# Performance work log

Measured on AMD Instinct MI355X. Metric: run time of the kernel, lower is better.

Reference implementation:

```python
import jax, jax.numpy as jnp
import numpy as np

N_NODES = 50000
N_EDGES = 800000
IN_DIM = 128
HIDDEN = 128
NUM_CLASSES = 64
NEG_SLOPE = 0.2


def setup_inputs() -> dict:
    key = jax.random.key(0)
    ks = jax.random.split(key, 12)
    x = jax.random.normal(ks[0], (N_NODES, IN_DIM), dtype=jnp.float32)
    src = jax.random.randint(ks[1], (N_EDGES,), 0, N_NODES, dtype=jnp.int64)
    dst = jax.random.randint(ks[2], (N_EDGES,), 0, N_NODES, dtype=jnp.int64)
    def glorot(k, shape):
        fan_in, fan_out = shape[0], shape[-1]
        s = jnp.sqrt(2.0 / (fan_in + fan_out)).astype(jnp.float32)
        return jax.random.normal(k, shape, dtype=jnp.float32) * s
    return {
        "x": x, "src": src, "dst": dst,
        # GATConv params (1 head, no bias, no residual)
        "W_gat": glorot(ks[3], (IN_DIM, HIDDEN)),
        "attn_l": glorot(ks[4], (HIDDEN,)),
        "attn_r": glorot(ks[5], (HIDDEN,)),
        # GraphConv params (norm='none', bias=True)
        "W1": glorot(ks[6], (HIDDEN, HIDDEN)),
        "b1": jnp.zeros((HIDDEN,), dtype=jnp.float32),
        "W2": glorot(ks[7], (HIDDEN, HIDDEN)),
        "b2": jnp.zeros((HIDDEN,), dtype=jnp.float32),
        "Wc": glorot(ks[8], (HIDDEN, NUM_CLASSES)),
        "bc": jnp.zeros((NUM_CLASSES,), dtype=jnp.float32),
    }


def reference(x, src, dst, W_gat, attn_l, attn_r, W1, b1, W2, b2, Wc, bc):
    N = x.shape[0]
    # --- GATConv, single head, eval mode (dropout=0) ---
    h = x @ W_gat                      # (N, H)
    el = h @ attn_l                    # (N,)
    er = h @ attn_r                    # (N,)
    e = jax.nn.leaky_relu(el[src] + er[dst], negative_slope=NEG_SLOPE)  # (E,)
    # edge softmax over incoming edges of each dst node
    emax = jax.ops.segment_max(e, dst, num_segments=N)
    ee = jnp.exp(e - emax[dst])
    esum = jax.ops.segment_sum(ee, dst, num_segments=N)
    alpha = ee / esum[dst]             # (E,) attention = reused edge weights
    h1 = jax.ops.segment_sum(h[src] * alpha[:, None], dst, num_segments=N)
    h1 = jax.nn.elu(h1)                # GATConv activation

    # --- GraphConv (norm='none') with edge_weight = alpha ---
    def gconv(hin, W, b):
        hp = hin @ W                                   # project (order is math-equivalent)
        agg = jax.ops.segment_sum(hp[src] * alpha[:, None], dst, num_segments=N)
        return agg + b

    h2 = gconv(h1, W1, b1)
    h3 = gconv(h2, W2, b2)
    logits = gconv(h3, Wc, bc)         # (N, num_classes)
    return logits
```

## Files before the change

### kernel.cpp

```cpp
#include <hip/hip_runtime.h>
#include <hip/hip_fp16.h>
#include <math.h>

#define N_NODES 50000
#define N_EDGES 800000
#define PAD_EDGES (N_EDGES + 8 * N_NODES)

typedef _Float16 half8 __attribute__((ext_vector_type(8)));
typedef float floatx16 __attribute__((ext_vector_type(16)));

__global__ __launch_bounds__(256) void prep_a_k(const float* __restrict__ Wg,
                                                const float* __restrict__ W1,
                                                const float* __restrict__ W2,
                                                const float* __restrict__ b1,
                                                __half* __restrict__ Wg_hl,
                                                float* __restrict__ W12,
                                                float* __restrict__ c12) {
  int e = blockIdx.x * 256 + threadIdx.x;
  if (e < 16384) {
    _Float16* o = (_Float16*)Wg_hl;
    int k = e >> 7, n = e & 127;
    float w = Wg[k * 128 + n];
    _Float16 hi = (_Float16)w;
    float lo = w - (float)hi;
    int oi = (((k >> 3) * 128 + n) << 3) | (k & 7);
    o[oi] = hi;
    o[16384 + oi] = (_Float16)lo;
  } else if (e < 32768) {
    int local = e - 16384;
    int k = local >> 7, n = local & 127;
    float acc = 0.f;
    for (int j = 0; j < 128; ++j) acc = fmaf(W1[k * 128 + j], W2[j * 128 + n], acc);
    W12[k * 128 + n] = acc;
  } else if (e < 32896) {
    int n = e - 32768;
    float acc = 0.f;
    for (int j = 0; j < 128; ++j) acc = fmaf(b1[j], W2[j * 128 + n], acc);
    c12[n] = acc;
  }
}

__global__ __launch_bounds__(256) void prepP_k(const float* __restrict__ W12,
                                               const float* __restrict__ c12,
                                               const float* __restrict__ Wc,
                                               const float* __restrict__ b2,
                                               __half* __restrict__ WPhl,
                                               float* __restrict__ c1,
                                               float* __restrict__ c2) {
  int e = blockIdx.x * 256 + threadIdx.x;
  _Float16* o = (_Float16*)WPhl;
  if (e < 8192) {
    int k = e >> 6, n = e & 63;
    float acc = 0.f;
    for (int j = 0; j < 128; ++j) acc = fmaf(W12[k * 128 + j], Wc[j * 64 + n], acc);
    _Float16 hi = (_Float16)acc;
    float lo = acc - (float)hi;
    int oi = (((k >> 3) * 64 + n) << 3) | (k & 7);
    o[oi] = hi;
    o[8192 + oi] = (_Float16)lo;
  } else if (e < 8256) {
    int n = e - 8192;
    float acc = 0.f;
    for (int j = 0; j < 128; ++j) acc = fmaf(c12[j], Wc[j * 64 + n], acc);
    c1[n] = acc;
  } else if (e < 8320) {
    int n = e - 8256;
    float acc = 0.f;
    for (int j = 0; j < 128; ++j) acc = fmaf(b2[j], Wc[j * 64 + n], acc);
    c2[n] = acc;
  }
}

template <int NCOL, bool A16, bool ELR>
__global__ __launch_bounds__(256) void mgemm_k(const void* __restrict__ Ap,
                                               const __half* __restrict__ Whl,
                                               __half* __restrict__ C16, int M,
                                               const float* __restrict__ al,
                                               const float* __restrict__ ar,
                                               float* __restrict__ el,
                                               float* __restrict__ er) {
  __shared__ __half Al[16][129][8];
  const int tid  = threadIdx.x;
  const int row0 = blockIdx.x * 128;
  const int lane = tid & 63;
  const int lane31 = lane & 31;
  const int q = lane >> 5;
  const int r = tid >> 6;

  if (A16) {
    const uint4* A8 = (const uint4*)Ap;
    #pragma unroll
    for (int i = 0; i < 8; ++i) {
      int idx = tid + i * 256;
      int row = idx >> 4, c = idx & 15;
      int grow = row0 + row;
      uint4 v = make_uint4(0u, 0u, 0u, 0u);
      if (grow < M) v = A8[grow * 16 + c];
      *reinterpret_cast<uint4*>(&Al[c][row][0]) = v;
    }
  } else {
    const float4* A4 = (const float4*)Ap;
    #pragma unroll
    for (int i = 0; i < 8; ++i) {
      int idx = tid + i * 256;
      int row = idx >> 4, c = idx & 15;
      int grow = row0 + row;
      half8 hv = {};
      if (grow < M) {
        float4 a0 = A4[grow * 32 + c * 2];
        float4 a1 = A4[grow * 32 + c * 2 + 1];
        hv[0] = (_Float16)a0.x; hv[1] = (_Float16)a0.y;
        hv[2] = (_Float16)a0.z; hv[3] = (_Float16)a0.w;
        hv[4] = (_Float16)a1.x; hv[5] = (_Float16)a1.y;
        hv[6] = (_Float16)a1.z; hv[7] = (_Float16)a1.w;
      }
      *reinterpret_cast<half8*>(&Al[c][row][0]) = hv;
    }
  }
  __syncthreads();

  half8 afr[8];
  #pragma unroll
  for (int s = 0; s < 8; ++s)
    afr[s] = *reinterpret_cast<const half8*>(&Al[2 * s + q][r * 32 + lane31][0]);

  const half8* B8 = reinterpret_cast<const half8*>(Whl);
  const int KN8 = 16 * NCOL;

  float elp[16], erp[16];
  if (ELR) {
    #pragma unroll
    for (int i = 0; i < 16; ++i) { elp[i] = 0.f; erp[i] = 0.f; }
  }

  #pragma unroll
  for (int tc = 0; tc < NCOL / 32; ++tc) {
    floatx16 acc = {};
    int nbase = tc * 32 + lane31;
    #pragma unroll
    for (int s = 0; s < 8; ++s) {
      int ci = (2 * s + q) * NCOL + nbase;
      half8 bl = B8[KN8 + ci];
      half8 bh = B8[ci];
      acc = __builtin_amdgcn_mfma_f32_32x32x16_f16(afr[s], bl, acc, 0, 0, 0);
      acc = __builtin_amdgcn_mfma_f32_32x32x16_f16(afr[s], bh, acc, 0, 0, 0);
    }
    if (ELR) {
      float alv = al[nbase], arv = ar[nbase];
      #pragma unroll
      for (int i = 0; i < 16; ++i) {
        elp[i] = fmaf(acc[i], alv, elp[i]);
        erp[i] = fmaf(acc[i], arv, erp[i]);
      }
    }
    #pragma unroll
    for (int i = 0; i < 16; ++i) {
      int rl = (i & 3) + 8 * (i >> 2) + 4 * q;
      int grow = row0 + r * 32 + rl;
      if (grow < M) C16[grow * NCOL + nbase] = __float2half(acc[i]);
    }
  }

  if (ELR) {
    #pragma unroll
    for (int off = 1; off <= 16; off <<= 1) {
      #pragma unroll
      for (int i = 0; i < 16; ++i) {
        elp[i] += __shfl_xor(elp[i], off);
        erp[i] += __shfl_xor(erp[i], off);
      }
    }
    if (lane31 == 0) {
      #pragma unroll
      for (int i = 0; i < 16; ++i) {
        int rl = (i & 3) + 8 * (i >> 2) + 4 * q;
        int grow = row0 + r * 32 + rl;
        if (grow < M) { el[grow] = elp[i]; er[grow] = erp[i]; }
      }
    }
  }
}

__global__ __launch_bounds__(256) void hist_k(const int* __restrict__ dst,
                                              int* __restrict__ deg,
                                              int* __restrict__ rank, int E) {
  int e = blockIdx.x * 256 + threadIdx.x;
  if (e < E) rank[e] = atomicAdd(&deg[dst[e]], 1);
}

__global__ __launch_bounds__(256) void scan1_k(const int* __restrict__ deg,
                                               int* __restrict__ offs,
                                               int* __restrict__ bsum, int N) {
  __shared__ int s[256];
  int t = threadIdx.x;
  int i = blockIdx.x * 256 + t;
  int v = 0;
  if (i < N) {
    int d = deg[i];
    v = (d + 7) & ~7;
    if (v < 8) v = 8;
  }
  s[t] = v;
  __syncthreads();
  for (int o = 1; o < 256; o <<= 1) {
    int add = (t >= o) ? s[t - o] : 0;
    __syncthreads();
    s[t] += add;
    __syncthreads();
  }
  if (i < N) offs[i] = s[t] - v;
  if (t == 255) bsum[blockIdx.x] = s[255];
}

__global__ __launch_bounds__(256) void scan2_k(int* __restrict__ bsum, int nb) {
  __shared__ int s[256];
  int t = threadIdx.x;
  int v = (t < nb) ? bsum[t] : 0;
  s[t] = v;
  __syncthreads();
  for (int o = 1; o < 256; o <<= 1) {
    int add = (t >= o) ? s[t - o] : 0;
    __syncthreads();
    s[t] += add;
    __syncthreads();
  }
  if (t < nb) bsum[t] = s[t] - v;
}

__global__ __launch_bounds__(256) void scan3_k(int* __restrict__ offs,
                                               const int* __restrict__ deg,
                                               const int* __restrict__ bsum,
                                               const float* __restrict__ el,
                                               float2* __restrict__ el2, int N) {
  int i = blockIdx.x * 256 + threadIdx.x;
  if (i < N) {
    int o = offs[i] + bsum[blockIdx.x];
    offs[i] = o;
    int d = deg[i];
    el2[i] = make_float2(el[i], (d > 0) ? 1.f : 0.f);
    if (i == N - 1) {
      int pd = (d + 7) & ~7;
      if (pd < 8) pd = 8;
      offs[N] = o + pd;
    }
  }
}

__global__ __launch_bounds__(256) void scatter_k(const int* __restrict__ src,
                                                 const int* __restrict__ dst,
                                                 const int* __restrict__ offs,
                                                 const int* __restrict__ rank,
                                                 int* __restrict__ csr_src, int E) {
  int e = blockIdx.x * 256 + threadIdx.x;
  if (e < E) {
    csr_src[offs[dst[e]] + rank[e]] = src[e];
  }
}

__device__ inline void fma8(float2 acc[4], uint4 u, float a) {
  __half2* h = reinterpret_cast<__half2*>(&u);
  #pragma unroll
  for (int j = 0; j < 4; ++j) {
    float2 f = __half22float2(h[j]);
    acc[j].x = fmaf(a, f.x, acc[j].x);
    acc[j].y = fmaf(a, f.y, acc[j].y);
  }
}

__global__ __launch_bounds__(256) void aggsm_k(const int* __restrict__ offs,
                                               const int* __restrict__ deg,
                                               const int* __restrict__ csr_src,
                                               const float2* __restrict__ el2,
                                               const float* __restrict__ er,
                                               int2* __restrict__ meta,
                                               float* __restrict__ t,
                                               const __half* __restrict__ hp,
                                               __half* __restrict__ out, int N) {
  __shared__ int2 lmeta[4][64];
  int wv   = threadIdx.x >> 6;
  int w    = (blockIdx.x * 256 + threadIdx.x) >> 6;
  int lane = threadIdx.x & 63;
  if (w >= N) return;
  int o0   = offs[w];
  int pcnt = offs[w + 1] - o0;
  int cnt  = deg[w];
  int q  = lane >> 4;
  int fl = lane & 15;
  const uint4* hpq = reinterpret_cast<const uint4*>(hp);

  if (cnt <= 64) {
    bool valid = lane < cnt;
    float erv = er[w];
    int s = 0;
    float ev = -3.4e38f, flag = 0.f;
    if (valid) {
      s = csr_src[o0 + lane];
      float2 e2 = el2[s];
      float e0 = e2.x + erv;
      ev = (e0 >= 0.f) ? e0 : 0.2f * e0;
      flag = e2.y;
    }
    float m = ev;
    #pragma unroll
    for (int off = 32; off; off >>= 1) m = fmaxf(m, __shfl_xor(m, off));
    float ee = valid ? __expf(ev - m) : 0.f;
    float sum = ee, tp = ee * flag;
    #pragma unroll
    for (int off = 32; off; off >>= 1) {
      sum += __shfl_xor(sum, off);
      tp  += __shfl_xor(tp, off);
    }
    float inv = (cnt > 0) ? 1.f / sum : 0.f;
    int2 mm = make_int2(0, 0);
    if (valid) mm = make_int2(s * 16, __float_as_int(ee * inv));
    if (lane < pcnt) meta[o0 + lane] = mm;
    lmeta[wv][lane] = mm;
    if (lane == 0) t[w] = tp * inv;
  } else {
    float erv = er[w];
    float m = -3.4e38f;
    for (int i = lane; i < cnt; i += 64) {
      int s = csr_src[o0 + i];
      float2 e2 = el2[s];
      float ev = e2.x + erv;
      ev = (ev >= 0.f) ? ev : 0.2f * ev;
      m = fmaxf(m, ev);
    }
    #pragma unroll
    for (int off = 32; off; off >>= 1) m = fmaxf(m, __shfl_xor(m, off));
    float sum = 0.f, tacc = 0.f;
    int myS = 0; float myE = 0.f;
    for (int i = lane; i < cnt; i += 64) {
      int s = csr_src[o0 + i];
      float2 e2 = el2[s];
      float ev = e2.x + erv;
      ev = (ev >= 0.f) ? ev : 0.2f * ev;
      float ee = __expf(ev - m);
      meta[o0 + i] = make_int2(s * 16, __float_as_int(ee));
      sum += ee;
      tacc += ee * e2.y;
      if (i == lane) { myS = s; myE = ee; }
    }
    #pragma unroll
    for (int off = 32; off; off >>= 1) {
      sum  += __shfl_xor(sum, off);
      tacc += __shfl_xor(tacc, off);
    }
    float inv = 1.f / sum;
    if (lane == 0) t[w] = tacc * inv;
    for (int i = lane; i < cnt; i += 64) {
      int2 mm = meta[o0 + i];
      meta[o0 + i] = make_int2(mm.x, __float_as_int(__int_as_float(mm.y) * inv));
    }
    for (int i = cnt + lane; i < pcnt; i += 64) meta[o0 + i] = make_int2(0, 0);
    lmeta[wv][lane] = make_int2(myS * 16, __float_as_int(myE * inv));
  }

  float2 acc0[4] = {}, acc1[4] = {};
  int pc = pcnt < 64 ? pcnt : 64;
  int2 mA = lmeta[wv][q], mB = lmeta[wv][4 + q];
  for (int base = 8; base < pc; base += 8) {
    int2 nA = lmeta[wv][base + q], nB = lmeta[wv][base + 4 + q];
    uint4 vA = hpq[mA.x + fl], vB = hpq[mB.x + fl];
    fma8(acc0, vA, __int_as_float(mA.y));
    fma8(acc1, vB, __int_as_float(mB.y));
    mA = nA; mB = nB;
  }
  {
    uint4 vA = hpq[mA.x + fl], vB = hpq[mB.x + fl];
    fma8(acc0, vA, __int_as_float(mA.y));
    fma8(acc1, vB, __int_as_float(mB.y));
  }
  for (int p = o0 + 64 + q; p < o0 + pcnt; p += 4) {
    int2 mm = meta[p];
    fma8(acc0, hpq[mm.x + fl], __int_as_float(mm.y));
  }
  #pragma unroll
  for (int j = 0; j < 4; ++j) { acc0[j].x += acc1[j].x; acc0[j].y += acc1[j].y; }
  #pragma unroll
  for (int off = 16; off <= 32; off <<= 1) {
    #pragma unroll
    for (int j = 0; j < 4; ++j) {
      acc0[j].x += __shfl_xor(acc0[j].x, off);
      acc0[j].y += __shfl_xor(acc0[j].y, off);
    }
  }
  if (q == 0) {
    float o8[8];
    #pragma unroll
    for (int j = 0; j < 4; ++j) { o8[2 * j] = acc0[j].x; o8[2 * j + 1] = acc0[j].y; }
    #pragma unroll
    for (int j = 0; j < 8; ++j) o8[j] = (o8[j] > 0.f) ? o8[j] : (__expf(o8[j]) - 1.f);
    __half2 p0 = __floats2half2_rn(o8[0], o8[1]);
    __half2 p1 = __floats2half2_rn(o8[2], o8[3]);
    __half2 p2 = __floats2half2_rn(o8[4], o8[5]);
    __half2 p3 = __floats2half2_rn(o8[6], o8[7]);
    uint4 pk;
    pk.x = *reinterpret_cast<unsigned*>(&p0);
    pk.y = *reinterpret_cast<unsigned*>(&p1);
    pk.z = *reinterpret_cast<unsigned*>(&p2);
    pk.w = *reinterpret_cast<unsigned*>(&p3);
    *reinterpret_cast<uint4*>(&out[w * 128 + fl * 8]) = pk;
  }
}

template <bool FINAL>
__global__ __launch_bounds__(256) void agg64v_k(const int* __restrict__ offs,
                                                const int2* __restrict__ meta,
                                                const __half* __restrict__ zp,
                                                const float* __restrict__ t,
                                                const int* __restrict__ deg,
                                                const float* __restrict__ c1,
                                                const float* __restrict__ c2,
                                                const float* __restrict__ bc,
                                                void* __restrict__ outp, int N) {
  int w    = (blockIdx.x * 256 + threadIdx.x) >> 6;
  int lane = threadIdx.x & 63;
  if (w >= N) return;
  int o0 = offs[w], o1 = offs[w + 1];
  int o   = lane >> 3;
  int fl  = lane & 7;
  const uint4* hpq = reinterpret_cast<const uint4*>(zp);

  float2 acc0[4] = {};
  int p = o0 + o;
  int2 mA = meta[p];
  for (; p + 8 < o1; p += 8) {
    int2 nA = meta[p + 8];
    uint4 vA = hpq[(mA.x >> 1) + fl];
    fma8(acc0, vA, __int_as_float(mA.y));
    mA = nA;
  }
  {
    uint4 vA = hpq[(mA.x >> 1) + fl];
    fma8(acc0, vA, __int_as_float(mA.y));
  }
  #pragma unroll
  for (int off = 8; off <= 32; off <<= 1) {
    #pragma unroll
    for (int j = 0; j < 4; ++j) {
      acc0[j].x += __shfl_xor(acc0[j].x, off);
      acc0[j].y += __shfl_xor(acc0[j].y, off);
    }
  }
  if (o == 0) {
    float o8[8];
    #pragma unroll
    for (int j = 0; j < 4; ++j) { o8[2 * j] = acc0[j].x; o8[2 * j + 1] = acc0[j].y; }
    if (FINAL) {
      float tw = t[w];
      float dw = (deg[w] > 0) ? 1.f : 0.f;
      float4 a0 = reinterpret_cast<const float4*>(c1)[fl * 2];
      float4 a1 = reinterpret_cast<const float4*>(c1)[fl * 2 + 1];
      float4 d0 = reinterpret_cast<const float4*>(c2)[fl * 2];
      float4 d1 = reinterpret_cast<const float4*>(c2)[fl * 2 + 1];
      float4 b0 = reinterpret_cast<const float4*>(bc)[fl * 2];
      float4 b1v = reinterpret_cast<const float4*>(bc)[fl * 2 + 1];
      o8[0] += tw * a0.x + dw * d0.x + b0.x;
      o8[1] += tw * a0.y + dw * d0.y + b0.y;
      o8[2] += tw * a0.z + dw * d0.z + b0.z;
      o8[3] += tw * a0.w + dw * d0.w + b0.w;
      o8[4] += tw * a1.x + dw * d1.x + b1v.x;
      o8[5] += tw * a1.y + dw * d1.y + b1v.y;
      o8[6] += tw * a1.z + dw * d1.z + b1v.z;
      o8[7] += tw * a1.w + dw * d1.w + b1v.w;
      float4* of = reinterpret_cast<float4*>(outp);
      of[w * 16 + fl * 2]     = make_float4(o8[0], o8[1], o8[2], o8[3]);
      of[w * 16 + fl * 2 + 1] = make_float4(o8[4], o8[5], o8[6], o8[7]);
    } else {
      __half2 p0 = __floats2half2_rn(o8[0], o8[1]);
      __half2 p1 = __floats2half2_rn(o8[2], o8[3]);
      __half2 p2 = __floats2half2_rn(o8[4], o8[5]);
      __half2 p3 = __floats2half2_rn(o8[6], o8[7]);
      uint4 pk;
      pk.x = *reinterpret_cast<unsigned*>(&p0);
      pk.y = *reinterpret_cast<unsigned*>(&p1);
      pk.z = *reinterpret_cast<unsigned*>(&p2);
      pk.w = *reinterpret_cast<unsigned*>(&p3);
      reinterpret_cast<uint4*>(outp)[w * 8 + fl] = pk;
    }
  }
}

extern "C" void kernel_launch(void* const* d_in, const int* in_sizes, int n_in,
                              void* d_out, int out_size, void* d_ws, size_t ws_size,
                              hipStream_t stream) {
  const float* x      = (const float*)d_in[0];
  const int*   src    = (const int*)d_in[1];
  const int*   dst    = (const int*)d_in[2];
  const float* W_gat  = (const float*)d_in[3];
  const float* attn_l = (const float*)d_in[4];
  const float* attn_r = (const float*)d_in[5];
  const float* W1     = (const float*)d_in[6];
  const float* b1     = (const float*)d_in[7];
  const float* W2     = (const float*)d_in[8];
  const float* b2     = (const float*)d_in[9];
  const float* Wc     = (const float*)d_in[10];
  const float* bc     = (const float*)d_in[11];
  float* out = (float*)d_out;

  char* ws = (char*)d_ws;
  size_t off = 0;
  auto walloc = [&](size_t bytes) -> void* {
    void* p = ws + off;
    off += (bytes + 255) & ~size_t(255);
    return p;
  };
  __half* P16     = (__half*)walloc((size_t)N_NODES * 128 * 2);
  __half* F16     = (__half*)walloc((size_t)N_NODES * 128 * 2);
  float*  el      = (float*)walloc((size_t)N_NODES * 4);
  float*  er      = (float*)walloc((size_t)N_NODES * 4);
  float2* el2     = (float2*)walloc((size_t)N_NODES * 8);
  float*  tbuf    = (float*)walloc((size_t)N_NODES * 4);
  int*    deg     = (int*)walloc((size_t)N_NODES * 4);
  int*    offs    = (int*)walloc((size_t)(N_NODES + 1) * 4);
  int*    rank    = (int*)walloc((size_t)N_EDGES * 4);
  int*    csr_src = (int*)walloc((size_t)PAD_EDGES * 4);
  int2*   meta    = (int2*)walloc((size_t)PAD_EDGES * 8);
  int*    bsum    = (int*)walloc(1024);
  __half* Wg_hl   = (__half*)walloc((size_t)32768 * 2);
  __half* WP_hl   = (__half*)walloc((size_t)16384 * 2);
  float*  W12     = (float*)walloc((size_t)16384 * 4);
  float*  c12     = (float*)walloc((size_t)128 * 4);
  float*  c1      = (float*)walloc((size_t)64 * 4);
  float*  c2      = (float*)walloc((size_t)64 * 4);

  hipMemsetAsync(deg, 0, (size_t)N_NODES * 4, stream);

  const dim3 blk(256);
  const int nwave_blocks = (N_NODES + 3) / 4;
  const int nedge_blocks = (N_EDGES + 255) / 256;
  const int nscan_blocks = (N_NODES + 255) / 256;
  const int ngemm_blocks = (N_NODES + 127) / 128;

  prep_a_k<<<dim3(129), blk, 0, stream>>>(W_gat, W1, W2, b1, Wg_hl, W12, c12);
  prepP_k<<<dim3(33), blk, 0, stream>>>(W12, c12, Wc, b2, WP_hl, c1, c2);

  mgemm_k<128, false, true><<<dim3(ngemm_blocks), blk, 0, stream>>>(
      x, Wg_hl, P16, N_NODES, attn_l, attn_r, el, er);

  hist_k<<<dim3(nedge_blocks), blk, 0, stream>>>(dst, deg, rank, N_EDGES);
  scan1_k<<<dim3(nscan_blocks), blk, 0, stream>>>(deg, offs, bsum, N_NODES);
  scan2_k<<<dim3(1), blk, 0, stream>>>(bsum, nscan_blocks);
  scan3_k<<<dim3(nscan_blocks), blk, 0, stream>>>(offs, deg, bsum, el, el2, N_NODES);
  scatter_k<<<dim3(nedge_blocks), blk, 0, stream>>>(src, dst, offs, rank, csr_src, N_EDGES);

  aggsm_k<<<dim3(nwave_blocks), blk, 0, stream>>>(offs, deg, csr_src, el2, er, meta, tbuf, P16, F16, N_NODES);
  mgemm_k<64, true, false><<<dim3(ngemm_blocks), blk, 0, stream>>>(
      F16, WP_hl, P16, N_NODES, nullptr, nullptr, nullptr, nullptr);
  agg64v_k<false><<<dim3(nwave_blocks), blk, 0, stream>>>(offs, meta, P16, nullptr, nullptr, nullptr, nullptr, nullptr, F16, N_NODES);
  agg64v_k<false><<<dim3(nwave_blocks), blk, 0, stream>>>(offs, meta, F16, nullptr, nullptr, nullptr, nullptr, nullptr, P16, N_NODES);
  agg64v_k<true><<<dim3(nwave_blocks), blk, 0, stream>>>(offs, meta, P16, tbuf, deg, c1, c2, bc, out, N_NODES);
}
```

Measured before the change: 289.0 us.

## Fuse weight prep and CSR build into one persistent kernel with grid barriers

Merges the two weight-prep kernels, histogram, three scan kernels and scatter into a single persistent kernel of 196 blocks that synchronises phases with atomic grid barriers, removing six kernel launches and their gaps. The el/degree-flag packing moves into the first GEMM epilogue, which now reads deg, so that GEMM must run after the CSR build. Per-node padding grows from 8 to 16 so agg64v can process two edges per lane per iteration with two accumulators for more memory-level parallelism. The grid barrier assumes all 196 blocks are co-resident, and the larger padding adds wasted zero-weight edge work.

```diff
diff --git a/kernel.cpp b/kernel.cpp
--- a/kernel.cpp
+++ b/kernel.cpp
@@ -4,71 +4,145 @@
 
 #define N_NODES 50000
 #define N_EDGES 800000
-#define PAD_EDGES (N_EDGES + 8 * N_NODES)
+#define PAD_EDGES (N_EDGES + 16 * N_NODES)
+#define NB_COOP 196
 
 typedef _Float16 half8 __attribute__((ext_vector_type(8)));
 typedef float floatx16 __attribute__((ext_vector_type(16)));
 
-__global__ __launch_bounds__(256) void prep_a_k(const float* __restrict__ Wg,
-                                                const float* __restrict__ W1,
-                                                const float* __restrict__ W2,
-                                                const float* __restrict__ b1,
-                                                __half* __restrict__ Wg_hl,
-                                                float* __restrict__ W12,
-                                                float* __restrict__ c12) {
-  int e = blockIdx.x * 256 + threadIdx.x;
-  if (e < 16384) {
-    _Float16* o = (_Float16*)Wg_hl;
-    int k = e >> 7, n = e & 127;
-    float w = Wg[k * 128 + n];
-    _Float16 hi = (_Float16)w;
-    float lo = w - (float)hi;
-    int oi = (((k >> 3) * 128 + n) << 3) | (k & 7);
-    o[oi] = hi;
-    o[16384 + oi] = (_Float16)lo;
-  } else if (e < 32768) {
-    int local = e - 16384;
-    int k = local >> 7, n = local & 127;
-    float acc = 0.f;
-    for (int j = 0; j < 128; ++j) acc = fmaf(W1[k * 128 + j], W2[j * 128 + n], acc);
-    W12[k * 128 + n] = acc;
-  } else if (e < 32896) {
-    int n = e - 32768;
-    float acc = 0.f;
-    for (int j = 0; j < 128; ++j) acc = fmaf(b1[j], W2[j * 128 + n], acc);
-    c12[n] = acc;
-  }
-}
-
-__global__ __launch_bounds__(256) void prepP_k(const float* __restrict__ W12,
-                                               const float* __restrict__ c12,
-                                               const float* __restrict__ Wc,
-                                               const float* __restrict__ b2,
-                                               __half* __restrict__ WPhl,
-                                               float* __restrict__ c1,
-                                               float* __restrict__ c2) {
-  int e = blockIdx.x * 256 + threadIdx.x;
-  _Float16* o = (_Float16*)WPhl;
-  if (e < 8192) {
-    int k = e >> 6, n = e & 63;
-    float acc = 0.f;
-    for (int j = 0; j < 128; ++j) acc = fmaf(W12[k * 128 + j], Wc[j * 64 + n], acc);
-    _Float16 hi = (_Float16)acc;
-    float lo = acc - (float)hi;
-    int oi = (((k >> 3) * 64 + n) << 3) | (k & 7);
-    o[oi] = hi;
-    o[8192 + oi] = (_Float16)lo;
-  } else if (e < 8256) {
-    int n = e - 8192;
-    float acc = 0.f;
-    for (int j = 0; j < 128; ++j) acc = fmaf(c12[j], Wc[j * 64 + n], acc);
-    c1[n] = acc;
-  } else if (e < 8320) {
-    int n = e - 8256;
-    float acc = 0.f;
-    for (int j = 0; j < 128; ++j) acc = fmaf(b2[j], Wc[j * 64 + n], acc);
-    c2[n] = acc;
-  }
+__device__ inline void gridbar(int* bar, int ph) {
+  __syncthreads();
+  if (threadIdx.x == 0) {
+    __hip_atomic_fetch_add(&bar[ph], 1, __ATOMIC_RELEASE, __HIP_MEMORY_SCOPE_AGENT);
+    while (__hip_atomic_load(&bar[ph], __ATOMIC_ACQUIRE, __HIP_MEMORY_SCOPE_AGENT) < NB_COOP)
+      __builtin_amdgcn_s_sleep(8);
+  }
+  __syncthreads();
+}
+
+__global__ __launch_bounds__(256) void coop_k(const int* __restrict__ src,
+                                              const int* __restrict__ dst,
+                                              const float* __restrict__ Wg,
+                                              const float* __restrict__ W1,
+                                              const float* __restrict__ W2,
+                                              const float* __restrict__ b1,
+                                              const float* __restrict__ Wc,
+                                              const float* __restrict__ b2,
+                                              int* __restrict__ deg,
+                                              int* __restrict__ rank,
+                                              int* __restrict__ offs,
+                                              int* __restrict__ csr_src,
+                                              int* __restrict__ bsum,
+                                              int* __restrict__ bsum2,
+                                              __half* __restrict__ Wg_hl,
+                                              float* __restrict__ W12,
+                                              float* __restrict__ c12,
+                                              __half* __restrict__ WPhl,
+                                              float* __restrict__ c1,
+                                              float* __restrict__ c2,
+                                              int* __restrict__ bar) {
+  __shared__ int s[256];
+  const int tid = threadIdx.x;
+  const int gt = blockIdx.x * 256 + tid;
+  const int GT = NB_COOP * 256;
+
+  for (int e = gt; e < 32896; e += GT) {
+    if (e < 16384) {
+      _Float16* o = (_Float16*)Wg_hl;
+      int k = e >> 7, n = e & 127;
+      float w = Wg[k * 128 + n];
+      _Float16 hi = (_Float16)w;
+      float lo = w - (float)hi;
+      int oi = (((k >> 3) * 128 + n) << 3) | (k & 7);
+      o[oi] = hi;
+      o[16384 + oi] = (_Float16)lo;
+    } else if (e < 32768) {
+      int local = e - 16384;
+      int k = local >> 7, n = local & 127;
+      float acc = 0.f;
+      for (int j = 0; j < 128; ++j) acc = fmaf(W1[k * 128 + j], W2[j * 128 + n], acc);
+      W12[k * 128 + n] = acc;
+    } else {
+      int n = e - 32768;
+      float acc = 0.f;
+      for (int j = 0; j < 128; ++j) acc = fmaf(b1[j], W2[j * 128 + n], acc);
+      c12[n] = acc;
+    }
+  }
+  gridbar(bar, 0);
+
+  for (int e = gt; e < N_EDGES; e += GT) rank[e] = atomicAdd(&deg[dst[e]], 1);
+  for (int e = gt; e < 8320; e += GT) {
+    _Float16* o = (_Float16*)WPhl;
+    if (e < 8192) {
+      int k = e >> 6, n = e & 63;
+      float acc = 0.f;
+      for (int j = 0; j < 128; ++j) acc = fmaf(W12[k * 128 + j], Wc[j * 64 + n], acc);
+      _Float16 hi = (_Float16)acc;
+      float lo = acc - (float)hi;
+      int oi = (((k >> 3) * 64 + n) << 3) | (k & 7);
+      o[oi] = hi;
+      o[8192 + oi] = (_Float16)lo;
+    } else if (e < 8256) {
+      int n = e - 8192;
+      float acc = 0.f;
+      for (int j = 0; j < 128; ++j) acc = fmaf(c12[j], Wc[j * 64 + n], acc);
+      c1[n] = acc;
+    } else {
+      int n = e - 8256;
+      float acc = 0.f;
+      for (int j = 0; j < 128; ++j) acc = fmaf(b2[j], Wc[j * 64 + n], acc);
+      c2[n] = acc;
+    }
+  }
+  gridbar(bar, 1);
+
+  const int i = gt;
+  int v = 0;
+  if (i < N_NODES) {
+    int d = deg[i];
+    v = (d + 15) & ~15;
+    if (v < 16) v = 16;
+  }
+  s[tid] = v;
+  __syncthreads();
+  for (int o = 1; o < 256; o <<= 1) {
+    int add = (tid >= o) ? s[tid - o] : 0;
+    __syncthreads();
+    s[tid] += add;
+    __syncthreads();
+  }
+  if (i < N_NODES) offs[i] = s[tid] - v;
+  if (tid == 255) bsum[blockIdx.x] = s[255];
+  gridbar(bar, 2);
+
+  if (blockIdx.x == 0) {
+    int bv = (tid < NB_COOP) ? bsum[tid] : 0;
+    s[tid] = bv;
+    __syncthreads();
+    for (int o = 1; o < 256; o <<= 1) {
+      int add = (tid >= o) ? s[tid - o] : 0;
+      __syncthreads();
+      s[tid] += add;
+      __syncthreads();
+    }
+    if (tid < NB_COOP) bsum2[tid] = s[tid] - bv;
+  }
+  gridbar(bar, 3);
+
+  if (i < N_NODES) {
+    int o = offs[i] + bsum2[blockIdx.x];
+    offs[i] = o;
+    if (i == N_NODES - 1) {
+      int d = deg[i];
+      int pd = (d + 15) & ~15;
+      if (pd < 16) pd = 16;
+      offs[N_NODES] = o + pd;
+    }
+  }
+  gridbar(bar, 4);
+
+  for (int e = gt; e < N_EDGES; e += GT) csr_src[offs[dst[e]] + rank[e]] = src[e];
 }
 
 template <int NCOL, bool A16, bool ELR>
@@ -77,8 +151,9 @@
                                                __half* __restrict__ C16, int M,
                                                const float* __restrict__ al,
                                                const float* __restrict__ ar,
-                                               float* __restrict__ el,
-                                               float* __restrict__ er) {
+                                               float2* __restrict__ el2,
+                                               float* __restrict__ er,
+                                               const int* __restrict__ deg) {
   __shared__ __half Al[16][129][8];
   const int tid  = threadIdx.x;
   const int row0 = blockIdx.x * 128;
@@ -175,85 +250,12 @@
       for (int i = 0; i < 16; ++i) {
         int rl = (i & 3) + 8 * (i >> 2) + 4 * q;
         int grow = row0 + r * 32 + rl;
-        if (grow < M) { el[grow] = elp[i]; er[grow] = erp[i]; }
+        if (grow < M) {
+          er[grow] = erp[i];
+          el2[grow] = make_float2(elp[i], (deg[grow] > 0) ? 1.f : 0.f);
+        }
       }
     }
-  }
-}
-
-__global__ __launch_bounds__(256) void hist_k(const int* __restrict__ dst,
-                                              int* __restrict__ deg,
-                                              int* __restrict__ rank, int E) {
-  int e = blockIdx.x * 256 + threadIdx.x;
-  if (e < E) rank[e] = atomicAdd(&deg[dst[e]], 1);
-}
-
-__global__ __launch_bounds__(256) void scan1_k(const int* __restrict__ deg,
-                                               int* __restrict__ offs,
-                                               int* __restrict__ bsum, int N) {
-  __shared__ int s[256];
-  int t = threadIdx.x;
-  int i = blockIdx.x * 256 + t;
-  int v = 0;
-  if (i < N) {
-    int d = deg[i];
-    v = (d + 7) & ~7;
-    if (v < 8) v = 8;
-  }
-  s[t] = v;
-  __syncthreads();
-  for (int o = 1; o < 256; o <<= 1) {
-    int add = (t >= o) ? s[t - o] : 0;
-    __syncthreads();
-    s[t] += add;
-    __syncthreads();
-  }
-  if (i < N) offs[i] = s[t] - v;
-  if (t == 255) bsum[blockIdx.x] = s[255];
-}
-
-__global__ __launch_bounds__(256) void scan2_k(int* __restrict__ bsum, int nb) {
-  __shared__ int s[256];
-  int t = threadIdx.x;
-  int v = (t < nb) ? bsum[t] : 0;
-  s[t] = v;
-  __syncthreads();
-  for (int o = 1; o < 256; o <<= 1) {
-    int add = (t >= o) ? s[t - o] : 0;
-    __syncthreads();
-    s[t] += add;
-    __syncthreads();
-  }
-  if (t < nb) bsum[t] = s[t] - v;
-}
-
-__global__ __launch_bounds__(256) void scan3_k(int* __restrict__ offs,
-                                               const int* __restrict__ deg,
-                                               const int* __restrict__ bsum,
-                                               const float* __restrict__ el,
-                                               float2* __restrict__ el2, int N) {
-  int i = blockIdx.x * 256 + threadIdx.x;
-  if (i < N) {
-    int o = offs[i] + bsum[blockIdx.x];
-    offs[i] = o;
-    int d = deg[i];
-    el2[i] = make_float2(el[i], (d > 0) ? 1.f : 0.f);
-    if (i == N - 1) {
-      int pd = (d + 7) & ~7;
-      if (pd < 8) pd = 8;
-      offs[N] = o + pd;
-    }
-  }
-}
-
-__global__ __launch_bounds__(256) void scatter_k(const int* __restrict__ src,
-                                                 const int* __restrict__ dst,
-                                                 const int* __restrict__ offs,
-                                                 const int* __restrict__ rank,
-                                                 int* __restrict__ csr_src, int E) {
-  int e = blockIdx.x * 256 + threadIdx.x;
-  if (e < E) {
-    csr_src[offs[dst[e]] + rank[e]] = src[e];
   }
 }
 
@@ -422,19 +424,25 @@
   int fl  = lane & 7;
   const uint4* hpq = reinterpret_cast<const uint4*>(zp);
 
-  float2 acc0[4] = {};
+  float2 acc0[4] = {}, acc1[4] = {};
   int p = o0 + o;
-  int2 mA = meta[p];
-  for (; p + 8 < o1; p += 8) {
-    int2 nA = meta[p + 8];
+  int2 mA = meta[p], mB = meta[p + 8];
+  for (; p + 16 < o1; p += 16) {
+    int2 nA = meta[p + 16], nB = meta[p + 24];
     uint4 vA = hpq[(mA.x >> 1) + fl];
+    uint4 vB = hpq[(mB.x >> 1) + fl];
     fma8(acc0, vA, __int_as_float(mA.y));
-    mA = nA;
+    fma8(acc1, vB, __int_as_float(mB.y));
+    mA = nA; mB = nB;
   }
   {
     uint4 vA = hpq[(mA.x >> 1) + fl];
+    uint4 vB = hpq[(mB.x >> 1) + fl];
     fma8(acc0, vA, __int_as_float(mA.y));
-  }
+    fma8(acc1, vB, __int_as_float(mB.y));
+  }
+  #pragma unroll
+  for (int j = 0; j < 4; ++j) { acc0[j].x += acc1[j].x; acc0[j].y += acc1[j].y; }
   #pragma unroll
   for (int off = 8; off <= 32; off <<= 1) {
     #pragma unroll
@@ -508,16 +516,17 @@
   };
   __half* P16     = (__half*)walloc((size_t)N_NODES * 128 * 2);
   __half* F16     = (__half*)walloc((size_t)N_NODES * 128 * 2);
-  float*  el      = (float*)walloc((size_t)N_NODES * 4);
   float*  er      = (float*)walloc((size_t)N_NODES * 4);
   float2* el2     = (float2*)walloc((size_t)N_NODES * 8);
   float*  tbuf    = (float*)walloc((size_t)N_NODES * 4);
-  int*    deg     = (int*)walloc((size_t)N_NODES * 4);
+  int*    deg     = (int*)walloc((size_t)N_NODES * 4 + 64);
+  int*    bar     = deg + N_NODES;
   int*    offs    = (int*)walloc((size_t)(N_NODES + 1) * 4);
   int*    rank    = (int*)walloc((size_t)N_EDGES * 4);
   int*    csr_src = (int*)walloc((size_t)PAD_EDGES * 4);
   int2*   meta    = (int2*)walloc((size_t)PAD_EDGES * 8);
   int*    bsum    = (int*)walloc(1024);
+  int*    bsum2   = (int*)walloc(1024);
   __half* Wg_hl   = (__half*)walloc((size_t)32768 * 2);
   __half* WP_hl   = (__half*)walloc((size_t)16384 * 2);
   float*  W12     = (float*)walloc((size_t)16384 * 4);
@@ -525,29 +534,22 @@
   float*  c1      = (float*)walloc((size_t)64 * 4);
   float*  c2      = (float*)walloc((size_t)64 * 4);
 
-  hipMemsetAsync(deg, 0, (size_t)N_NODES * 4, stream);
+  hipMemsetAsync(deg, 0, (size_t)N_NODES * 4 + 64, stream);
 
   const dim3 blk(256);
   const int nwave_blocks = (N_NODES + 3) / 4;
-  const int nedge_blocks = (N_EDGES + 255) / 256;
-  const int nscan_blocks = (N_NODES + 255) / 256;
   const int ngemm_blocks = (N_NODES + 127) / 128;
 
-  prep_a_k<<<dim3(129), blk, 0, stream>>>(W_gat, W1, W2, b1, Wg_hl, W12, c12);
-  prepP_k<<<dim3(33), blk, 0, stream>>>(W12, c12, Wc, b2, WP_hl, c1, c2);
+  coop_k<<<dim3(NB_COOP), blk, 0, stream>>>(src, dst, W_gat, W1, W2, b1, Wc, b2,
+                                            deg, rank, offs, csr_src, bsum, bsum2,
+                                            Wg_hl, W12, c12, WP_hl, c1, c2, bar);
 
   mgemm_k<128, false, true><<<dim3(ngemm_blocks), blk, 0, stream>>>(
-      x, Wg_hl, P16, N_NODES, attn_l, attn_r, el, er);
-
-  hist_k<<<dim3(nedge_blocks), blk, 0, stream>>>(dst, deg, rank, N_EDGES);
-  scan1_k<<<dim3(nscan_blocks), blk, 0, stream>>>(deg, offs, bsum, N_NODES);
-  scan2_k<<<dim3(1), blk, 0, stream>>>(bsum, nscan_blocks);
-  scan3_k<<<dim3(nscan_blocks), blk, 0, stream>>>(offs, deg, bsum, el, el2, N_NODES);
-  scatter_k<<<dim3(nedge_blocks), blk, 0, stream>>>(src, dst, offs, rank, csr_src, N_EDGES);
+      x, Wg_hl, P16, N_NODES, attn_l, attn_r, el2, er, deg);
 
   aggsm_k<<<dim3(nwave_blocks), blk, 0, stream>>>(offs, deg, csr_src, el2, er, meta, tbuf, P16, F16, N_NODES);
   mgemm_k<64, true, false><<<dim3(ngemm_blocks), blk, 0, stream>>>(
-      F16, WP_hl, P16, N_NODES, nullptr, nullptr, nullptr, nullptr);
+      F16, WP_hl, P16, N_NODES, nullptr, nullptr, nullptr, nullptr, nullptr);
   agg64v_k<false><<<dim3(nwave_blocks), blk, 0, stream>>>(offs, meta, P16, nullptr, nullptr, nullptr, nullptr, nullptr, F16, N_NODES);
   agg64v_k<false><<<dim3(nwave_blocks), blk, 0, stream>>>(offs, meta, F16, nullptr, nullptr, nullptr, nullptr, nullptr, P16, N_NODES);
   agg64v_k<true><<<dim3(nwave_blocks), blk, 0, stream>>>(offs, meta, P16, tbuf, deg, c1, c2, bc, out, N_NODES);
```

New measurement: 333.2 us. +15.3%, slower.
